# Kernel tuning notes

Hardware: AMD Instinct MI355X
Metric: run time of the kernel (lower is better)

## Reference

```python
import jax, jax.numpy as jnp
import numpy as np

N_E = 8192
E_DIM = 64
BETA = 0.25
N_TOKENS = 32768


def setup_inputs() -> dict:
    key = jax.random.key(0)
    k1, k2 = jax.random.split(key)
    x = jax.random.normal(k1, (N_TOKENS, E_DIM), dtype=jnp.float32)
    # nn.Embedding weight initialized uniform(-1/n_e, 1/n_e)
    codebook = jax.random.uniform(k2, (N_E, E_DIM), dtype=jnp.float32,
                                  minval=-1.0 / N_E, maxval=1.0 / N_E)
    return {"x": x, "codebook": codebook, "start": 0, "end": N_E, "use_sk": 0}


def reference(x, codebook, start, end, use_sk):
    # use_sk=0 -> argmin branch (sinkhorn branch calls external helper, not exercised)
    latent = x.reshape(-1, E_DIM)                       # [N, D]
    cb = codebook[start:end]                            # [K, D]
    # squared euclidean distances: ||z||^2 + ||e||^2 - 2 z.e
    d = (jnp.sum(latent * latent, axis=1, keepdims=True)
         + jnp.sum(cb * cb, axis=1)[None, :]
         - 2.0 * jnp.einsum('nd,kd->nk', latent, cb))   # [N, K]
    indices = jnp.argmin(d, axis=-1) + start            # [N]
    x_q = codebook[indices].reshape(x.shape)            # gather
    sg = jax.lax.stop_gradient
    commitment_loss = jnp.mean((sg(x_q) - x) ** 2)
    codebook_loss = jnp.mean((x_q - sg(x)) ** 2)
    loss = codebook_loss + BETA * commitment_loss
    x_q_st = x + sg(x_q - x)                            # straight-through estimator
    indices = indices.reshape(x.shape[:-1])
    return x_q_st, loss, indices
```

## Files before the change

### kernel.cpp

```cpp
#include <hip/hip_runtime.h>
#include <math.h>


#define N_E    8192
#define EDIM   64
#define NTOK   32768
#define NELEM  (NTOK * EDIM)
#define CSZ    32
#define WINDOW 3e-4f
#define TTOK   128
#define TCODE  1024
#define SROW   72
#define TOKB   16
#define CCAP   64
#define KCAP   320

typedef __attribute__((ext_vector_type(8)))  short          short8;
typedef __attribute__((ext_vector_type(8)))  unsigned short ushort8v;
typedef __attribute__((ext_vector_type(16))) float          f32x16;

__device__ __forceinline__ unsigned short f2bf(float f) {
  unsigned int u = __float_as_uint(f);
  return (unsigned short)((u + 0x7FFFu + ((u >> 16) & 1u)) >> 16);
}
__device__ __forceinline__ unsigned short f2h(float f) {
  union { _Float16 h; unsigned short u; } cv; cv.h = (_Float16)f; return cv.u;
}
__device__ __forceinline__ float h2f(unsigned short b) {
  union { _Float16 h; unsigned short u; } cv; cv.u = b; return (float)cv.h;
}
__device__ __forceinline__ float max16(const f32x16 a) {
  float m = fmaxf(fmaxf(a[0], a[1]), a[2]);
  m = fmaxf(fmaxf(m, a[3]),  a[4]);
  m = fmaxf(fmaxf(m, a[5]),  a[6]);
  m = fmaxf(fmaxf(m, a[7]),  a[8]);
  m = fmaxf(fmaxf(m, a[9]),  a[10]);
  m = fmaxf(fmaxf(m, a[11]), a[12]);
  m = fmaxf(fmaxf(m, a[13]), a[14]);
  return fmaxf(m, a[15]);
}
__device__ __forceinline__ float sx_of(const float4* xl4) {
#pragma clang fp contract(off)
  float a0=0,a1=0,a2=0,a3=0,a4=0,a5=0,a6=0,a7=0;
#pragma unroll
  for (int i = 0; i < 8; ++i) {
    float4 pA = xl4[2*i], pB = xl4[2*i+1];
    a0 += pA.x * pA.x; a1 += pA.y * pA.y; a2 += pA.z * pA.z; a3 += pA.w * pA.w;
    a4 += pB.x * pB.x; a5 += pB.y * pB.y; a6 += pB.z * pB.z; a7 += pB.w * pB.w;
  }
  return ((a0+a1) + (a2+a3)) + ((a4+a5) + (a6+a7));
}

__global__ __launch_bounds__(256) void vq_sc(const float* __restrict__ cb,
                                             float* __restrict__ sc,
                                             unsigned short* __restrict__ cbf) {
#pragma clang fp contract(off)
  int r = blockIdx.x * 256 + threadIdx.x;
  const float4* c4 = (const float4*)(cb + (size_t)r * EDIM);
  float sval = sx_of(c4);
  sc[r] = sval;
  unsigned short* dst = cbf + (size_t)r * EDIM;
#pragma unroll
  for (int h = 0; h < 8; ++h) {
    float4 fA = c4[2*h], fB = c4[2*h+1];
    ushort8v o = {f2bf(fA.x), f2bf(fA.y), f2bf(fA.z), f2bf(fA.w),
                  f2bf(fB.x), f2bf(fB.y), f2bf(fB.z), f2bf(fB.w)};
    *(ushort8v*)&dst[h * 8] = o;
  }
}

__global__ __launch_bounds__(256, 4) void vq_pass1(
    const float* __restrict__ x, const unsigned short* __restrict__ cbf,
    unsigned int* __restrict__ cand, unsigned int* __restrict__ bmapb,
    const int* __restrict__ p_start, const int* __restrict__ p_end) {
  __shared__ unsigned short Cs[128 * SROW];
  int tid = threadIdx.x;
  int tb = blockIdx.x;
  int cbk = blockIdx.y;
  int s = *p_start, e = *p_end;
  const bool allfull = (cbk * TCODE >= s) && (cbk * TCODE + TCODE <= e);

  int lane = tid & 63, wv = tid >> 6;
  int half = lane >> 5, ln = lane & 31;
  int tokbase = wv * 32;

  const ushort8v* cg0 = (const ushort8v*)(cbf + (size_t)cbk * TCODE * EDIM);
#pragma unroll
  for (int p = 0; p < 4; ++p) {
    int idx = tid + p * 256;
    int row = idx >> 3, h = idx & 7;
    *(ushort8v*)&Cs[row * SROW + h * 8] = cg0[idx];
  }

  short8 bfr[4];
  {
    const float* xrow =
        x + (size_t)(tb * TTOK + tokbase + ln) * EDIM + half * 8;
#pragma unroll
    for (int ks = 0; ks < 4; ++ks) {
      float4 fA = *(const float4*)(xrow + ks * 16);
      float4 fB = *(const float4*)(xrow + ks * 16 + 4);
      short8 v = {(short)f2bf(fA.x), (short)f2bf(fA.y), (short)f2bf(fA.z),
                  (short)f2bf(fA.w), (short)f2bf(fB.x), (short)f2bf(fB.y),
                  (short)f2bf(fB.z), (short)f2bf(fB.w)};
      bfr[ks] = v;
    }
  }
  __syncthreads();

  unsigned s0=~0u,s1=~0u,s2=~0u,s3=~0u,s4=~0u,s5=~0u,s6=~0u,s7=~0u,s8=~0u;
  unsigned m0=0,m1=0,m2=0,m3=0,m4=0,m5=0,m6=0,m7=0,m8=0;
  unsigned bmap = 0u;
  float lm = INFINITY;

  for (int nb = 0; nb < 8; ++nb) {
    ushort8v creg[4];
    if (nb < 7) {
      const ushort8v* cg =
          (const ushort8v*)(cbf + ((size_t)cbk * TCODE + (nb + 1) * 128) * EDIM);
#pragma unroll
      for (int p = 0; p < 4; ++p) creg[p] = cg[tid + p * 256];
    }
#pragma unroll
    for (int cp = 0; cp < 2; ++cp) {
      f32x16 acc[2];
#pragma unroll
      for (int c2 = 0; c2 < 2; ++c2) acc[c2] = (f32x16)0.0f;
#pragma unroll
      for (int ks = 0; ks < 4; ++ks)
#pragma unroll
        for (int c2 = 0; c2 < 2; ++c2) {
          int ct = cp * 2 + c2;
          short8 a = *(const short8*)&Cs[(ct*32 + ln) * SROW + ks*16 + half*8];
          acc[c2] = __builtin_amdgcn_mfma_f32_32x32x16_bf16(a, bfr[ks],
                                                            acc[c2], 0, 0, 0);
        }
#pragma unroll
      for (int c2 = 0; c2 < 2; ++c2) {
        int cidL = nb * 4 + cp * 2 + c2;
        float v;
        if (allfull) {
          v = max16(acc[c2]);
        } else {
          int c0 = cbk * TCODE + cidL * 32;
          bool full = (c0 >= s) && (c0 + 32 <= e);
          if (full) {
            v = max16(acc[c2]);
          } else {
            v = -INFINITY;
#pragma unroll
            for (int r = 0; r < 16; ++r) {
              int code = c0 + (r & 3) + 8 * (r >> 2) + 4 * half;
              if (code >= s && code < e) v = fmaxf(v, acc[c2][r]);
            }
          }
        }
        v = fmaxf(v, __shfl_xor(v, 32, 64));
        unsigned short hh = f2h(-2.0f * v);
        float mv = h2f(hh);
        lm = fminf(lm, mv);
        if (mv <= lm + WINDOW) {
          bmap |= 1u << cidL;
          float t = v - WINDOW * 0.5f;
          unsigned b = 0;
#pragma unroll
          for (int r = 0; r < 16; ++r) {
            int pos = (r & 3) + 8 * (r >> 2) + 4 * half;
            if (acc[c2][r] >= t) b |= (1u << pos);
          }
          b |= __shfl_xor(b, 32, 64);
          unsigned mono = (unsigned)hh ^ ((hh & 0x8000u) ? 0xFFFFu : 0x8000u);
          unsigned p = (mono << 16) | (unsigned)cidL;
          unsigned pm = b;
          if (p < s8) {
#define INS2_(SK, SM) { bool lt_ = p < (SK); unsigned tk_ = (SK), tm_ = (SM); \
            if (lt_) { (SK) = p; (SM) = pm; p = tk_; pm = tm_; } }
            INS2_(s0,m0) INS2_(s1,m1) INS2_(s2,m2) INS2_(s3,m3) INS2_(s4,m4)
            INS2_(s5,m5) INS2_(s6,m6) INS2_(s7,m7) INS2_(s8,m8)
#undef INS2_
          }
        }
      }
    }
    __syncthreads();
    if (nb < 7) {
#pragma unroll
      for (int p = 0; p < 4; ++p) {
        int idx = tid + p * 256;
        int row = idx >> 3, h = idx & 7;
        *(ushort8v*)&Cs[row * SROW + h * 8] = creg[p];
      }
    }
    __syncthreads();
  }

  if (!half) {
    float thr = lm + WINDOW;
    unsigned rec[8], msk[8];
#define EMIT_(J, S, M) { unsigned mono_ = (S) >> 16; \
    unsigned hh_ = (mono_ & 0x8000u) ? (mono_ ^ 0x8000u) : (mono_ ^ 0xFFFFu); \
    float v_ = h2f((unsigned short)hh_); \
    rec[J] = (v_ <= thr) ? ((hh_ << 16) | ((S) & 0xFFFFu)) : 0xFFFFFFFFu; \
    msk[J] = (M); }
    EMIT_(0, s0, m0) EMIT_(1, s1, m1) EMIT_(2, s2, m2) EMIT_(3, s3, m3)
    EMIT_(4, s4, m4) EMIT_(5, s5, m5) EMIT_(6, s6, m6) EMIT_(7, s7, m7)
#undef EMIT_
    {
      unsigned mono_ = s8 >> 16;
      unsigned hh_ = (mono_ & 0x8000u) ? (mono_ ^ 0x8000u) : (mono_ ^ 0xFFFFu);
      float v8 = h2f((unsigned short)hh_);
      if (v8 <= thr) rec[7] |= 0x8000u;
    }
    int tl = tokbase + ln;
    unsigned* eb = (unsigned*)Cs;
#pragma unroll
    for (int j = 0; j < 8; ++j) {
      eb[tl * 17 + j]     = rec[j];
      eb[tl * 17 + 8 + j] = msk[j];
    }
    bmapb[(size_t)cbk * NTOK + (tb * TTOK + tl)] = bmap;
  }
  __syncthreads();
#pragma unroll
  for (int p = 0; p < 2; ++p) {
    int idx = tid + p * 256;
    int tl = idx >> 2, part = idx & 3;
    const unsigned* src = (const unsigned*)Cs + tl * 17 + part * 4;
    uint4 v; v.x = src[0]; v.y = src[1]; v.z = src[2]; v.w = src[3];
    *(uint4*)(cand + (((size_t)(tb * TTOK + tl)) * 8 + cbk) * 16 + part * 4) = v;
  }
}

__global__ __launch_bounds__(256) void vq_rescue(
    const float* __restrict__ x, const float* __restrict__ cb,
    const float* __restrict__ sc, const unsigned int* __restrict__ cand,
    const unsigned int* __restrict__ bmapb,
    float* __restrict__ out_xq, float* __restrict__ out_idx,
    float* __restrict__ partial,
    const int* __restrict__ p_start, const int* __restrict__ p_end) {
#pragma clang fp contract(off)
  __shared__ float xsh[TOKB][64];
  __shared__ float sxs[TOKB];
  __shared__ unsigned short lst[TOKB][CCAP];
  __shared__ unsigned short clst[TOKB][KCAP];
  __shared__ int ccnt[TOKB], kcnt[TOKB];
  int tid  = threadIdx.x;
  int wv   = tid >> 6;
  int lane = tid & 63;
  int blk  = blockIdx.x;
  int s = *p_start, e = *p_end;

  if (tid < TOKB) { ccnt[tid] = 0; kcnt[tid] = 0; }
#pragma unroll
  for (int p = 0; p < (TOKB * CCAP) / 256; ++p)
    ((unsigned short*)lst)[tid + p * 256] = 0xFFFFu;
  __syncthreads();

  if (tid < 128) {
    int tl = tid >> 3, q = tid & 7;
    int gtok = blk * TOKB + tl;
    const uint4* rp = (const uint4*)(cand + ((size_t)gtok * 8 + q) * 16);
    uint4 A0 = rp[0], A1 = rp[1], M0 = rp[2], M1 = rp[3];
    unsigned rv[8] = {A0.x, A0.y, A0.z, A0.w, A1.x, A1.y, A1.z, A1.w};
    unsigned mk[8] = {M0.x, M0.y, M0.z, M0.w, M1.x, M1.y, M1.z, M1.w};
    float m = INFINITY;
#pragma unroll
    for (int j = 0; j < 8; ++j)
      m = fminf(m, h2f((unsigned short)(rv[j] >> 16)));
    m = fminf(m, __shfl_xor(m, 1, 64));
    m = fminf(m, __shfl_xor(m, 2, 64));
    m = fminf(m, __shfl_xor(m, 4, 64));
    float thr = m + WINDOW;
    bool marker = (rv[7] != 0xFFFFFFFFu) && ((rv[7] & 0x8000u) != 0u);
    unsigned slotbits = 0u;
#pragma unroll
    for (int j = 0; j < 8; ++j) {
      if (rv[j] != 0xFFFFFFFFu) {
        unsigned cid = rv[j] & 0x1Fu;
        slotbits |= 1u << cid;
        if (h2f((unsigned short)(rv[j] >> 16)) <= thr) {
          unsigned bits = mk[j];
          int n = __popc(bits);
          int base = atomicAdd(&ccnt[tl], n);
          if (base + n <= CCAP) {
            int kb = (q * 32 + (int)cid) * CSZ;
            while (bits) {
              int bpos = __ffs(bits) - 1; bits &= bits - 1;
              lst[tl][base++] = (unsigned short)(kb + bpos);
            }
          } else {
            int kb2 = atomicAdd(&kcnt[tl], 1);
            if (kb2 < KCAP) clst[tl][kb2] = (unsigned short)(q * 32 + (int)cid);
          }
        }
      }
    }
    if (marker) {
      unsigned bm = bmapb[(size_t)q * NTOK + gtok] & ~slotbits;
      int n = __popc(bm);
      int base = atomicAdd(&kcnt[tl], n);
      while (bm) {
        int j = __ffs(bm) - 1; bm &= bm - 1;
        if (base < KCAP) clst[tl][base] = (unsigned short)(q * 32 + j);
        ++base;
      }
    }
  } else if (tid < 192) {
    int t = tid - 128;
#pragma unroll
    for (int p = 0; p < 4; ++p) {
      int idx = t + p * 64;
      int tl = idx >> 4, seg = idx & 15;
      *(float4*)&xsh[tl][seg * 4] =
          ((const float4*)(x + (size_t)(blk * TOKB + tl) * EDIM))[seg];
    }
  } else if (tid < 192 + TOKB) {
    int tl = tid - 192;
    sxs[tl] = sx_of((const float4*)(x + (size_t)(blk * TOKB + tl) * EDIM));
  }
  __syncthreads();

#define EVAL_CODE_BODY(K_, XL4) do {                                           \
    const float4* c4_ = (const float4*)(cb + (size_t)(K_) * EDIM);             \
    float t0_=0.0f,t1_=0.0f,t2_=0.0f,t3_=0.0f;                                 \
    _Pragma("unroll")                                                          \
    for (int i_ = 0; i_ < 8; ++i_) {                 \
      float4 v_ = c4_[2*i_ + h5_];                                             \
      float4 p_ = (XL4)[2*i_ + h5_];                                           \
      t0_ += v_.x * p_.x; t1_ += v_.y * p_.y;                                  \
      t2_ += v_.z * p_.z; t3_ += v_.w * p_.w;                                  \
    }                                                                          \
    s2_ = (t0_ + t1_) + (t2_ + t3_);              \
  } while (0)

#define FINISH_CODE(K_, ACT, SX, BP) do {                                      \
    float tt_ = s2_ + __shfl_xor(s2_, 1, 64);                                  \
    if ((ACT) && (K_) >= s && (K_) < e) {                                      \
      float d_ = ((SX) + sc[K_]) - 2.0f * tt_;                                 \
      unsigned db_ = __float_as_uint(d_);                                      \
      unsigned en_ = db_ ^ ((unsigned)((int)db_ >> 31) | 0x80000000u);         \
      unsigned long long pk_ = ((unsigned long long)en_ << 32) | (unsigned)(K_);\
      if (pk_ < (BP)) (BP) = pk_;                                              \
    }                                                                          \
  } while (0)

  float sg[4];
#pragma unroll
  for (int ti = 0; ti < 4; ++ti) {
    int tl = wv * 4 + ti;
    int gtok = blk * TOKB + tl;
    const float4* xl4 = (const float4*)xsh[tl];
    float sx = sxs[tl];
    unsigned long long bp = ~0ull;
    int ci_ = lane >> 1, h5_ = lane & 1;
    int nc = ccnt[tl]; if (nc > CCAP) nc = CCAP;
    for (int b0 = 0; b0 < nc; b0 += 32) {
      int nb = nc - b0; if (nb > 32) nb = 32;
      int kraw = (ci_ < nb) ? (int)lst[tl][b0 + ci_] : 0xFFFF;
      bool act = (kraw != 0xFFFF);
      int k_ = act ? kraw : 0;
      float s2_ = 0.0f;
      if (act) EVAL_CODE_BODY(k_, xl4);
      FINISH_CODE(k_, act, sx, bp);
    }
    int nk = kcnt[tl]; if (nk > KCAP) nk = KCAP;
    for (int i = 0; i < nk; ++i) {
      int k_ = (int)clst[tl][i] * CSZ + ci_;
      float s2_;
      EVAL_CODE_BODY(k_, xl4);
      FINISH_CODE(k_, true, sx, bp);
    }
#pragma unroll
    for (int off = 32; off >= 1; off >>= 1) {
      unsigned long long o = __shfl_xor(bp, off, 64);
      if (o < bp) bp = o;
    }
    int bidx = (int)(unsigned)(bp & 0xFFFFFFFFull) & (N_E - 1);

    float xx = xsh[tl][lane];
    float qv = cb[(size_t)bidx * EDIM + lane];
    float diff = qv - xx;
    out_xq[(size_t)gtok * EDIM + lane] = xx + diff;
    if (lane == 0) out_idx[gtok] = (float)bidx;
    float l = diff * diff;
#pragma unroll
    for (int off = 32; off >= 1; off >>= 1) l += __shfl_down(l, off, 64);
    sg[ti] = l;
  }
#undef EVAL_CODE_BODY
#undef FINISH_CODE
  if (lane == 0)
    partial[blk * 4 + wv] = (sg[0] + sg[1]) + (sg[2] + sg[3]);
}

__global__ __launch_bounds__(256) void vq_loss(const float* __restrict__ partial,
                                               float* __restrict__ out_loss) {
  int tid = threadIdx.x;
  float s = 0.0f;
  for (int i = tid; i < NTOK / 4; i += 256) s += partial[i];
#pragma unroll
  for (int off = 32; off >= 1; off >>= 1) s += __shfl_down(s, off, 64);
  __shared__ float sdata[4];
  if ((tid & 63) == 0) sdata[tid >> 6] = s;
  __syncthreads();
  if (tid == 0) {
    float total = (sdata[0] + sdata[1]) + (sdata[2] + sdata[3]);
    float m = total * (1.0f / (float)NELEM);
    out_loss[0] = m + 0.25f * m;
  }
}

extern "C" void kernel_launch(void* const* d_in, const int* in_sizes, int n_in,
                              void* d_out, int out_size, void* d_ws, size_t ws_size,
                              hipStream_t stream) {
  const float* x  = (const float*)d_in[0];
  const float* cb = (const float*)d_in[1];
  const int* p_start = (const int*)d_in[2];
  const int* p_end   = (const int*)d_in[3];

  float* ws = (float*)d_ws;
  float* sc      = ws;
  float* partial = ws + N_E;
  unsigned short* cbf  = (unsigned short*)(ws + 2 * N_E);
  unsigned int*   cand = (unsigned int*)(cbf + (size_t)N_E * EDIM);
  unsigned int*   bmapb = cand + (size_t)NTOK * 8 * 16;

  float* out      = (float*)d_out;
  float* out_xq   = out;
  float* out_loss = out + NELEM;
  float* out_idx  = out + NELEM + 1;

  vq_sc<<<N_E / 256, 256, 0, stream>>>(cb, sc, cbf);
  dim3 g1(NTOK / TTOK, N_E / TCODE);
  vq_pass1<<<g1, 256, 0, stream>>>(x, cbf, cand, bmapb, p_start, p_end);
  vq_rescue<<<NTOK / TOKB, 256, 0, stream>>>(x, cb, sc, cand, bmapb, out_xq, out_idx,
                                             partial, p_start, p_end);
  vq_loss<<<1, 256, 0, stream>>>(partial, out_loss);
}
```

Baseline: 181.2 us.

## Split rescue kernel into candidate-parse and evaluation kernels via global lists

The rescue kernel is split into two launches. The first parses candidate records and bitmaps into per-token code lists and counts, which it writes to workspace. The second loads x, reads those lists from global memory and does the exact fp32 distance evaluation. This removes the large shared-memory list arrays from the evaluation kernel, which may raise occupancy. The cost is an extra launch plus a global write and read of the lists.

After: 187.3 us. 1.03x slower.

```diff
diff --git a/kernel.cpp b/kernel.cpp
--- a/kernel.cpp
+++ b/kernel.cpp
@@ -231,24 +231,16 @@
   }
 }
 
-__global__ __launch_bounds__(256) void vq_rescue(
-    const float* __restrict__ x, const float* __restrict__ cb,
-    const float* __restrict__ sc, const unsigned int* __restrict__ cand,
-    const unsigned int* __restrict__ bmapb,
-    float* __restrict__ out_xq, float* __restrict__ out_idx,
-    float* __restrict__ partial,
+__global__ __launch_bounds__(256) void vq_parse(
+    const unsigned int* __restrict__ cand, const unsigned int* __restrict__ bmapb,
+    unsigned int* __restrict__ gcnt, unsigned short* __restrict__ glst,
+    unsigned short* __restrict__ gclst,
     const int* __restrict__ p_start, const int* __restrict__ p_end) {
-#pragma clang fp contract(off)
-  __shared__ float xsh[TOKB][64];
-  __shared__ float sxs[TOKB];
   __shared__ unsigned short lst[TOKB][CCAP];
   __shared__ unsigned short clst[TOKB][KCAP];
   __shared__ int ccnt[TOKB], kcnt[TOKB];
-  int tid  = threadIdx.x;
-  int wv   = tid >> 6;
-  int lane = tid & 63;
-  int blk  = blockIdx.x;
-  int s = *p_start, e = *p_end;
+  int tid = threadIdx.x;
+  int blk = blockIdx.x;
 
   if (tid < TOKB) { ccnt[tid] = 0; kcnt[tid] = 0; }
 #pragma unroll
@@ -305,19 +297,54 @@
         ++base;
       }
     }
-  } else if (tid < 192) {
-    int t = tid - 128;
-#pragma unroll
-    for (int p = 0; p < 4; ++p) {
-      int idx = t + p * 64;
-      int tl = idx >> 4, seg = idx & 15;
-      *(float4*)&xsh[tl][seg * 4] =
-          ((const float4*)(x + (size_t)(blk * TOKB + tl) * EDIM))[seg];
-    }
-  } else if (tid < 192 + TOKB) {
-    int tl = tid - 192;
-    sxs[tl] = sx_of((const float4*)(x + (size_t)(blk * TOKB + tl) * EDIM));
-  }
+  }
+  __syncthreads();
+
+  if (tid < TOKB) {
+    int kc = kcnt[tid]; if (kc > KCAP) kc = KCAP;
+    gcnt[blk * TOKB + tid] = (unsigned)ccnt[tid] | ((unsigned)kc << 16);
+  }
+  if (tid < 128) {
+    int tl = tid >> 3, part = tid & 7;
+    *(uint4*)(glst + ((size_t)(blk * TOKB + tl)) * CCAP + part * 8) =
+        *(const uint4*)&lst[tl][part * 8];
+  } else {
+    int t2 = tid - 128;
+    int tl = t2 >> 3, p0 = t2 & 7;
+#pragma unroll
+    for (int p = 0; p < 5; ++p) {
+      int part = p0 + p * 8;
+      if (part * 8 < kcnt[tl] && part < 40)
+        *(uint4*)(gclst + ((size_t)(blk * TOKB + tl)) * KCAP + part * 8) =
+            *(const uint4*)&clst[tl][part * 8];
+    }
+  }
+}
+
+__global__ __launch_bounds__(256) void vq_eval(
+    const float* __restrict__ x, const float* __restrict__ cb,
+    const float* __restrict__ sc, const unsigned int* __restrict__ gcnt,
+    const unsigned short* __restrict__ glst, const unsigned short* __restrict__ gclst,
+    float* __restrict__ out_xq, float* __restrict__ out_idx,
+    float* __restrict__ partial,
+    const int* __restrict__ p_start, const int* __restrict__ p_end) {
+#pragma clang fp contract(off)
+  __shared__ float xsh[TOKB][64];
+  __shared__ float sxs[TOKB];
+  int tid  = threadIdx.x;
+  int wv   = tid >> 6;
+  int lane = tid & 63;
+  int blk  = blockIdx.x;
+  int s = *p_start, e = *p_end;
+
+  {
+    int ti = lane >> 4, seg = lane & 15;
+    int tl = wv * 4 + ti;
+    *(float4*)&xsh[tl][seg * 4] =
+        ((const float4*)(x + (size_t)(blk * TOKB + tl) * EDIM))[seg];
+  }
+  __syncthreads();
+  if (tid < TOKB) sxs[tid] = sx_of((const float4*)xsh[tid]);
   __syncthreads();
 
 #define EVAL_CODE_BODY(K_, XL4) do {                                           \
@@ -351,21 +378,22 @@
     int gtok = blk * TOKB + tl;
     const float4* xl4 = (const float4*)xsh[tl];
     float sx = sxs[tl];
+    unsigned cw = gcnt[gtok];
+    int nc = (int)(cw & 0xFFFFu); if (nc > CCAP) nc = CCAP;
+    int nk = (int)(cw >> 16);     if (nk > KCAP) nk = KCAP;
     unsigned long long bp = ~0ull;
     int ci_ = lane >> 1, h5_ = lane & 1;
-    int nc = ccnt[tl]; if (nc > CCAP) nc = CCAP;
     for (int b0 = 0; b0 < nc; b0 += 32) {
       int nb = nc - b0; if (nb > 32) nb = 32;
-      int kraw = (ci_ < nb) ? (int)lst[tl][b0 + ci_] : 0xFFFF;
+      int kraw = (ci_ < nb) ? (int)glst[(size_t)gtok * CCAP + b0 + ci_] : 0xFFFF;
       bool act = (kraw != 0xFFFF);
       int k_ = act ? kraw : 0;
       float s2_ = 0.0f;
       if (act) EVAL_CODE_BODY(k_, xl4);
       FINISH_CODE(k_, act, sx, bp);
     }
-    int nk = kcnt[tl]; if (nk > KCAP) nk = KCAP;
     for (int i = 0; i < nk; ++i) {
-      int k_ = (int)clst[tl][i] * CSZ + ci_;
+      int k_ = (int)gclst[(size_t)gtok * KCAP + i] * CSZ + ci_;
       float s2_;
       EVAL_CODE_BODY(k_, xl4);
       FINISH_CODE(k_, true, sx, bp);
@@ -424,6 +452,9 @@
   unsigned short* cbf  = (unsigned short*)(ws + 2 * N_E);
   unsigned int*   cand = (unsigned int*)(cbf + (size_t)N_E * EDIM);
   unsigned int*   bmapb = cand + (size_t)NTOK * 8 * 16;
+  unsigned int*   gcnt  = bmapb + (size_t)NTOK * 8;
+  unsigned short* glst  = (unsigned short*)(gcnt + NTOK);
+  unsigned short* gclst = glst + (size_t)NTOK * CCAP;
 
   float* out      = (float*)d_out;
   float* out_xq   = out;
@@ -433,7 +464,10 @@
   vq_sc<<<N_E / 256, 256, 0, stream>>>(cb, sc, cbf);
   dim3 g1(NTOK / TTOK, N_E / TCODE);
   vq_pass1<<<g1, 256, 0, stream>>>(x, cbf, cand, bmapb, p_start, p_end);
-  vq_rescue<<<NTOK / TOKB, 256, 0, stream>>>(x, cb, sc, cand, bmapb, out_xq, out_idx,
-                                             partial, p_start, p_end);
+  vq_parse<<<NTOK / TOKB, 256, 0, stream>>>(cand, bmapb, gcnt, glst, gclst,
+                                            p_start, p_end);
+  vq_eval<<<NTOK / TOKB, 256, 0, stream>>>(x, cb, sc, gcnt, glst, gclst,
+                                           out_xq, out_idx, partial,
+                                           p_start, p_end);
   vq_loss<<<1, 256, 0, stream>>>(partial, out_loss);
 }
```

## Replace per-token sorted candidate list with per-chunk fp16 max table

Applied to the files above, without the earlier changes.

The bf16 MFMA pass no longer keeps a register-resident sorted top-9 list with per-code bitmasks and a block map. Instead it writes the fp16-encoded best score of every 32-code chunk to shared memory and emits all 256 chunk scores per token. The rescue kernel then picks every chunk within the window of the global minimum and re-evaluates those chunks exactly in fp32. This removes the insertion sort and mask building from the hot loop. In exchange, rescue may evaluate more full chunks per token, and the KCAP=256 cap could drop candidates if many chunks fall in the window.

After: 178.8 us. About the same (-1.3%).

```diff
diff --git a/kernel.cpp b/kernel.cpp
--- a/kernel.cpp
+++ b/kernel.cpp
@@ -12,8 +12,7 @@
 #define TCODE  1024
 #define SROW   72
 #define TOKB   16
-#define CCAP   64
-#define KCAP   320
+#define KCAP   256
 
 typedef __attribute__((ext_vector_type(8)))  short          short8;
 typedef __attribute__((ext_vector_type(8)))  unsigned short ushort8v;
@@ -71,9 +70,10 @@
 
 __global__ __launch_bounds__(256, 4) void vq_pass1(
     const float* __restrict__ x, const unsigned short* __restrict__ cbf,
-    unsigned int* __restrict__ cand, unsigned int* __restrict__ bmapb,
+    unsigned int* __restrict__ cand,
     const int* __restrict__ p_start, const int* __restrict__ p_end) {
   __shared__ unsigned short Cs[128 * SROW];
+  __shared__ unsigned minL[128 * 17];
   int tid = threadIdx.x;
   int tb = blockIdx.x;
   int cbk = blockIdx.y;
@@ -108,10 +108,7 @@
   }
   __syncthreads();
 
-  unsigned s0=~0u,s1=~0u,s2=~0u,s3=~0u,s4=~0u,s5=~0u,s6=~0u,s7=~0u,s8=~0u;
-  unsigned m0=0,m1=0,m2=0,m3=0,m4=0,m5=0,m6=0,m7=0,m8=0;
-  unsigned bmap = 0u;
-  float lm = INFINITY;
+  unsigned short* minL16 = (unsigned short*)minL;
 
   for (int nb = 0; nb < 8; ++nb) {
     ushort8v creg[4];
@@ -156,30 +153,8 @@
           }
         }
         v = fmaxf(v, __shfl_xor(v, 32, 64));
-        unsigned short hh = f2h(-2.0f * v);
-        float mv = h2f(hh);
-        lm = fminf(lm, mv);
-        if (mv <= lm + WINDOW) {
-          bmap |= 1u << cidL;
-          float t = v - WINDOW * 0.5f;
-          unsigned b = 0;
-#pragma unroll
-          for (int r = 0; r < 16; ++r) {
-            int pos = (r & 3) + 8 * (r >> 2) + 4 * half;
-            if (acc[c2][r] >= t) b |= (1u << pos);
-          }
-          b |= __shfl_xor(b, 32, 64);
-          unsigned mono = (unsigned)hh ^ ((hh & 0x8000u) ? 0xFFFFu : 0x8000u);
-          unsigned p = (mono << 16) | (unsigned)cidL;
-          unsigned pm = b;
-          if (p < s8) {
-#define INS2_(SK, SM) { bool lt_ = p < (SK); unsigned tk_ = (SK), tm_ = (SM); \
-            if (lt_) { (SK) = p; (SM) = pm; p = tk_; pm = tm_; } }
-            INS2_(s0,m0) INS2_(s1,m1) INS2_(s2,m2) INS2_(s3,m3) INS2_(s4,m4)
-            INS2_(s5,m5) INS2_(s6,m6) INS2_(s7,m7) INS2_(s8,m8)
-#undef INS2_
-          }
-        }
+        if (!half)
+          minL16[(tokbase + ln) * 34 + cidL] = f2h(-2.0f * v);
       }
     }
     __syncthreads();
@@ -194,38 +169,11 @@
     __syncthreads();
   }
 
-  if (!half) {
-    float thr = lm + WINDOW;
-    unsigned rec[8], msk[8];
-#define EMIT_(J, S, M) { unsigned mono_ = (S) >> 16; \
-    unsigned hh_ = (mono_ & 0x8000u) ? (mono_ ^ 0x8000u) : (mono_ ^ 0xFFFFu); \
-    float v_ = h2f((unsigned short)hh_); \
-    rec[J] = (v_ <= thr) ? ((hh_ << 16) | ((S) & 0xFFFFu)) : 0xFFFFFFFFu; \
-    msk[J] = (M); }
-    EMIT_(0, s0, m0) EMIT_(1, s1, m1) EMIT_(2, s2, m2) EMIT_(3, s3, m3)
-    EMIT_(4, s4, m4) EMIT_(5, s5, m5) EMIT_(6, s6, m6) EMIT_(7, s7, m7)
-#undef EMIT_
-    {
-      unsigned mono_ = s8 >> 16;
-      unsigned hh_ = (mono_ & 0x8000u) ? (mono_ ^ 0x8000u) : (mono_ ^ 0xFFFFu);
-      float v8 = h2f((unsigned short)hh_);
-      if (v8 <= thr) rec[7] |= 0x8000u;
-    }
-    int tl = tokbase + ln;
-    unsigned* eb = (unsigned*)Cs;
-#pragma unroll
-    for (int j = 0; j < 8; ++j) {
-      eb[tl * 17 + j]     = rec[j];
-      eb[tl * 17 + 8 + j] = msk[j];
-    }
-    bmapb[(size_t)cbk * NTOK + (tb * TTOK + tl)] = bmap;
-  }
-  __syncthreads();
 #pragma unroll
   for (int p = 0; p < 2; ++p) {
     int idx = tid + p * 256;
     int tl = idx >> 2, part = idx & 3;
-    const unsigned* src = (const unsigned*)Cs + tl * 17 + part * 4;
+    const unsigned* src = minL + tl * 17 + part * 4;
     uint4 v; v.x = src[0]; v.y = src[1]; v.z = src[2]; v.w = src[3];
     *(uint4*)(cand + (((size_t)(tb * TTOK + tl)) * 8 + cbk) * 16 + part * 4) = v;
   }
@@ -234,75 +182,51 @@
 __global__ __launch_bounds__(256) void vq_rescue(
     const float* __restrict__ x, const float* __restrict__ cb,
     const float* __restrict__ sc, const unsigned int* __restrict__ cand,
-    const unsigned int* __restrict__ bmapb,
     float* __restrict__ out_xq, float* __restrict__ out_idx,
     float* __restrict__ partial,
     const int* __restrict__ p_start, const int* __restrict__ p_end) {
 #pragma clang fp contract(off)
   __shared__ float xsh[TOKB][64];
   __shared__ float sxs[TOKB];
-  __shared__ unsigned short lst[TOKB][CCAP];
   __shared__ unsigned short clst[TOKB][KCAP];
-  __shared__ int ccnt[TOKB], kcnt[TOKB];
+  __shared__ int kcnt[TOKB];
   int tid  = threadIdx.x;
   int wv   = tid >> 6;
   int lane = tid & 63;
   int blk  = blockIdx.x;
   int s = *p_start, e = *p_end;
 
-  if (tid < TOKB) { ccnt[tid] = 0; kcnt[tid] = 0; }
-#pragma unroll
-  for (int p = 0; p < (TOKB * CCAP) / 256; ++p)
-    ((unsigned short*)lst)[tid + p * 256] = 0xFFFFu;
+  if (tid < TOKB) kcnt[tid] = 0;
   __syncthreads();
 
   if (tid < 128) {
     int tl = tid >> 3, q = tid & 7;
     int gtok = blk * TOKB + tl;
     const uint4* rp = (const uint4*)(cand + ((size_t)gtok * 8 + q) * 16);
-    uint4 A0 = rp[0], A1 = rp[1], M0 = rp[2], M1 = rp[3];
-    unsigned rv[8] = {A0.x, A0.y, A0.z, A0.w, A1.x, A1.y, A1.z, A1.w};
-    unsigned mk[8] = {M0.x, M0.y, M0.z, M0.w, M1.x, M1.y, M1.z, M1.w};
+    uint4 A0 = rp[0], A1 = rp[1], A2 = rp[2], A3 = rp[3];
+    unsigned rw[16] = {A0.x, A0.y, A0.z, A0.w, A1.x, A1.y, A1.z, A1.w,
+                       A2.x, A2.y, A2.z, A2.w, A3.x, A3.y, A3.z, A3.w};
     float m = INFINITY;
 #pragma unroll
-    for (int j = 0; j < 8; ++j)
-      m = fminf(m, h2f((unsigned short)(rv[j] >> 16)));
+    for (int j = 0; j < 16; ++j) {
+      unsigned u = rw[j];
+      m = fminf(m, fminf(h2f((unsigned short)(u & 0xFFFFu)),
+                         h2f((unsigned short)(u >> 16))));
+    }
     m = fminf(m, __shfl_xor(m, 1, 64));
     m = fminf(m, __shfl_xor(m, 2, 64));
     m = fminf(m, __shfl_xor(m, 4, 64));
     float thr = m + WINDOW;
-    bool marker = (rv[7] != 0xFFFFFFFFu) && ((rv[7] & 0x8000u) != 0u);
-    unsigned slotbits = 0u;
-#pragma unroll
-    for (int j = 0; j < 8; ++j) {
-      if (rv[j] != 0xFFFFFFFFu) {
-        unsigned cid = rv[j] & 0x1Fu;
-        slotbits |= 1u << cid;
-        if (h2f((unsigned short)(rv[j] >> 16)) <= thr) {
-          unsigned bits = mk[j];
-          int n = __popc(bits);
-          int base = atomicAdd(&ccnt[tl], n);
-          if (base + n <= CCAP) {
-            int kb = (q * 32 + (int)cid) * CSZ;
-            while (bits) {
-              int bpos = __ffs(bits) - 1; bits &= bits - 1;
-              lst[tl][base++] = (unsigned short)(kb + bpos);
-            }
-          } else {
-            int kb2 = atomicAdd(&kcnt[tl], 1);
-            if (kb2 < KCAP) clst[tl][kb2] = (unsigned short)(q * 32 + (int)cid);
-          }
-        }
+#pragma unroll
+    for (int j = 0; j < 16; ++j) {
+      unsigned u = rw[j];
+      if (h2f((unsigned short)(u & 0xFFFFu)) <= thr) {
+        int i = atomicAdd(&kcnt[tl], 1);
+        if (i < KCAP) clst[tl][i] = (unsigned short)(q * 32 + 2 * j);
       }
-    }
-    if (marker) {
-      unsigned bm = bmapb[(size_t)q * NTOK + gtok] & ~slotbits;
-      int n = __popc(bm);
-      int base = atomicAdd(&kcnt[tl], n);
-      while (bm) {
-        int j = __ffs(bm) - 1; bm &= bm - 1;
-        if (base < KCAP) clst[tl][base] = (unsigned short)(q * 32 + j);
-        ++base;
+      if (h2f((unsigned short)(u >> 16)) <= thr) {
+        int i = atomicAdd(&kcnt[tl], 1);
+        if (i < KCAP) clst[tl][i] = (unsigned short)(q * 32 + 2 * j + 1);
       }
     }
   } else if (tid < 192) {
@@ -353,16 +277,6 @@
     float sx = sxs[tl];
     unsigned long long bp = ~0ull;
     int ci_ = lane >> 1, h5_ = lane & 1;
-    int nc = ccnt[tl]; if (nc > CCAP) nc = CCAP;
-    for (int b0 = 0; b0 < nc; b0 += 32) {
-      int nb = nc - b0; if (nb > 32) nb = 32;
-      int kraw = (ci_ < nb) ? (int)lst[tl][b0 + ci_] : 0xFFFF;
-      bool act = (kraw != 0xFFFF);
-      int k_ = act ? kraw : 0;
-      float s2_ = 0.0f;
-      if (act) EVAL_CODE_BODY(k_, xl4);
-      FINISH_CODE(k_, act, sx, bp);
-    }
     int nk = kcnt[tl]; if (nk > KCAP) nk = KCAP;
     for (int i = 0; i < nk; ++i) {
       int k_ = (int)clst[tl][i] * CSZ + ci_;
@@ -423,7 +337,6 @@
   float* partial = ws + N_E;
   unsigned short* cbf  = (unsigned short*)(ws + 2 * N_E);
   unsigned int*   cand = (unsigned int*)(cbf + (size_t)N_E * EDIM);
-  unsigned int*   bmapb = cand + (size_t)NTOK * 8 * 16;
 
   float* out      = (float*)d_out;
   float* out_xq   = out;
@@ -432,8 +345,8 @@
 
   vq_sc<<<N_E / 256, 256, 0, stream>>>(cb, sc, cbf);
   dim3 g1(NTOK / TTOK, N_E / TCODE);
-  vq_pass1<<<g1, 256, 0, stream>>>(x, cbf, cand, bmapb, p_start, p_end);
-  vq_rescue<<<NTOK / TOKB, 256, 0, stream>>>(x, cb, sc, cand, bmapb, out_xq, out_idx,
+  vq_pass1<<<g1, 256, 0, stream>>>(x, cbf, cand, p_start, p_end);
+  vq_rescue<<<NTOK / TOKB, 256, 0, stream>>>(x, cb, sc, cand, out_xq, out_idx,
                                              partial, p_start, p_end);
   vq_loss<<<1, 256, 0, stream>>>(partial, out_loss);
 }
```
